# Kernel tuning notes

Hardware: AMD Instinct MI355X
Metric: run time of the kernel (lower is better)

The kernel has to match this reference:

```python
import jax, jax.numpy as jnp
import numpy as np

DIM = 256; NH = 8; WH = 8; WW = 8; N = WH * WW
B, T, M, H, W = 2, 4, 5, 64, 64
HD = DIM // NH
SCALE = HD ** -0.5

def _rel_pos_index():
    coords = np.stack(np.meshgrid(np.arange(WH), np.arange(WW), indexing='ij'))
    cf = coords.reshape(2, -1)
    rc = (cf[:, :, None] - cf[:, None, :]).transpose(1, 2, 0)
    rc[:, :, 0] += WH - 1
    rc[:, :, 1] += WW - 1
    rc[:, :, 0] *= 2 * WW - 1
    return rc.sum(-1)  # (N, N) ints in [0, (2WH-1)(2WW-1))

RPI = _rel_pos_index()

def layer_norm(x, g, b, eps=1e-5):
    mu = x.mean(-1, keepdims=True)
    var = jnp.mean((x - mu) ** 2, axis=-1, keepdims=True)
    return (x - mu) * jax.lax.rsqrt(var + eps) * g + b

def setup_inputs():
    key = jax.random.key(0)
    ks = jax.random.split(key, 32)
    C = DIM
    w = lambda i, shape, s=0.02: jax.random.normal(ks[i], shape, jnp.float32) * s
    return {
        'x': jax.random.normal(ks[0], (B, T, H, W, C), jnp.float32),
        'kv': jax.random.normal(ks[1], (B, M, H, W, C), jnp.float32),
        'mask_matrix': jnp.zeros(((H // WH) * (W // WW), N, N), jnp.float32),
        'norm_q_g': jnp.ones((C,), jnp.float32), 'norm_q_b': jnp.zeros((C,), jnp.float32),
        'norm_kv_g': jnp.ones((C,), jnp.float32), 'norm_kv_b': jnp.zeros((C,), jnp.float32),
        'q_w': w(2, (C, C)), 'q_b': w(3, (C,)),
        'kv_w': w(4, (2 * C, C)), 'kv_b': w(5, (2 * C,)),
        'rpb_table': w(6, ((2 * WH - 1) * (2 * WW - 1), NH)),
        'pos_emb': jax.random.normal(ks[7], (N, C), jnp.float32) / C ** 0.5,
        'pq_w': w(8, (C, C)), 'pq_b': w(9, (C,)),
        'pk_w': w(10, (C, C)), 'pk_b': w(11, (C,)),
        'pv_w': w(12, (C, C)), 'pv_b': w(13, (C,)),
        'po_w': w(14, (C, C)), 'po_b': w(15, (C,)),
        'proj_w': w(16, (C, C)), 'proj_b': w(17, (C,)),
        'norm2_g': jnp.ones((C,), jnp.float32), 'norm2_b': jnp.zeros((C,), jnp.float32),
        'mlp_w1': w(18, (4 * C, C)), 'mlp_b1': w(19, (4 * C,)),
        'mlp_w2': w(20, (C, 4 * C)), 'mlp_b2': w(21, (C,)),
    }

def _attention_pool(xw, pos_emb, pq_w, pq_b, pk_w, pk_b, pv_w, pv_b, po_w, po_b):
    # CLIP-style attention pooling: xw (b, M, N, C) -> (b, N, C)
    b, m, n, C = xw.shape
    avg = xw.mean(axis=1, keepdims=True)
    xw = jnp.concatenate([avg, xw], axis=1) + pos_emb[None, None]  # (b, M+1, N, C)
    tok = xw.reshape(b, (m + 1) * n, C)  # flattened (m n) token axis
    q = (tok[:, :n] @ pq_w.T + pq_b).reshape(b, n, NH, HD).transpose(0, 2, 1, 3) * HD ** -0.5
    k = (tok @ pk_w.T + pk_b).reshape(b, -1, NH, HD).transpose(0, 2, 1, 3)
    v = (tok @ pv_w.T + pv_b).reshape(b, -1, NH, HD).transpose(0, 2, 1, 3)
    a = jax.nn.softmax(jnp.einsum('bhqd,bhkd->bhqk', q, k), axis=-1)
    o = jnp.einsum('bhqk,bhkd->bhqd', a, v).transpose(0, 2, 1, 3).reshape(b, n, C)
    return o @ po_w.T + po_b

def reference(x, kv, mask_matrix, norm_q_g, norm_q_b, norm_kv_g, norm_kv_b,
              q_w, q_b, kv_w, kv_b, rpb_table, pos_emb,
              pq_w, pq_b, pk_w, pk_b, pv_w, pv_b, po_w, po_b,
              proj_w, proj_b, norm2_g, norm2_b, mlp_w1, mlp_b1, mlp_w2, mlp_b2):
    Bv, Tv, Hv, Wv, C = x.shape
    Mv = kv.shape[1]
    nWh, nWw = Hv // WH, Wv // WW
    nW = nWh * nWw
    B_ = Bv * nW
    shortcut = x
    xq = layer_norm(x, norm_q_g, norm_q_b)
    xk = layer_norm(kv, norm_kv_g, norm_kv_b)

    def part(z, S):  # window partition (B,S,H,W,C) -> (B*nW, S, N, C)
        z = z.reshape(Bv, S, nWh, WH, nWw, WW, C)
        return z.transpose(0, 2, 4, 1, 3, 5, 6).reshape(B_, S, N, C)

    qw = part(xq, Tv)
    kvw = part(xk, Mv)
    q = (qw @ q_w.T + q_b).reshape(B_, Tv, N, NH, HD).transpose(0, 1, 3, 2, 4)   # (B_,T,h,N,d)
    kvp = (kvw @ kv_w.T + kv_b).reshape(B_, Mv, N, 2, NH, HD)
    k = kvp[:, :, :, 0].transpose(0, 1, 3, 2, 4)                                  # (B_,M,h,N,d)
    v = kvp[:, :, :, 1].transpose(0, 1, 3, 2, 4)
    attn = jnp.einsum('bthnd,bmhkd->btmhnk', q * SCALE, k)                        # (B_,T,M,h,N,N)
    rpb = rpb_table[RPI.reshape(-1)].reshape(N, N, NH).transpose(2, 0, 1)         # (h,N,N)
    attn = jax.nn.softmax(attn + rpb[None, None, None], axis=-1)  # shift=(0,0) -> mask_matrix unused
    out = jnp.einsum('btmhnk,bmhkd->btmhnd', attn, v)                             # (B_,T,M,h,N,d)
    # faithful to torch: transpose(1,2) (swap T/M) then flat reshape to (B_,T,M,N,C)
    out = out.transpose(0, 2, 1, 3, 4, 5).reshape(B_, Tv, Mv, N, C)
    out = out.reshape(B_ * Tv, Mv, N, C)
    out = _attention_pool(out, pos_emb, pq_w, pq_b, pk_w, pk_b, pv_w, pv_b, po_w, po_b)
    out = out.reshape(B_, Tv, N, C)
    out = jax.nn.gelu(out, approximate=False)
    out = out @ proj_w.T + proj_b
    # window reverse -> (B,T,H,W,C)
    out = out.reshape(Bv, nWh, nWw, Tv, WH, WW, C).transpose(0, 3, 1, 4, 2, 5, 6).reshape(Bv, Tv, Hv, Wv, C)
    x1 = shortcut + out
    h = layer_norm(x1, norm2_g, norm2_b)
    h = jax.nn.gelu(h @ mlp_w1.T + mlp_b1, approximate=False) @ mlp_w2.T + mlp_b2
    return x1 + h
```

## Files before the change

kernel.cpp:

```cpp
#include <hip/hip_runtime.h>
#include <hip/hip_bf16.h>
#include <cstddef>
#include <cstdint>

#define SCALE_QK 0.17677669529663687f

typedef __attribute__((ext_vector_type(8))) short bf16x8;
typedef __attribute__((ext_vector_type(4))) float f32x4;

__global__ __launch_bounds__(256) void convb_kernel(
    const float* __restrict__ src, __hip_bfloat16* __restrict__ dst, int n) {
  int i = blockIdx.x * 256 + threadIdx.x;
  if (i < n) dst[i] = __float2bfloat16(src[i]);
}

__global__ __launch_bounds__(256) void ln_part_kernel(
    const float* __restrict__ in, __hip_bfloat16* __restrict__ out,
    const float* __restrict__ gamma, const float* __restrict__ beta,
    int S, int b0) {
  int r = blockIdx.x;
  int n = r & 63;
  int tmp = r >> 6;
  int s = tmp % S;
  int b_ = b0 + tmp / S;
  int b  = b_ >> 6;
  int wh = (b_ >> 3) & 7;
  int ww = b_ & 7;
  int gh = wh * 8 + (n >> 3);
  int gw = ww * 8 + (n & 7);
  const float* src = in + (((size_t)(b * S + s) * 64 + gh) * 64 + gw) * 256;
  int c = threadIdx.x;
  float v = src[c];
  __shared__ float red[256];
  red[c] = v; __syncthreads();
  for (int off = 128; off > 0; off >>= 1) { if (c < off) red[c] += red[c + off]; __syncthreads(); }
  float mu = red[0] * (1.f / 256.f);
  __syncthreads();
  float dv = v - mu;
  red[c] = dv * dv; __syncthreads();
  for (int off = 128; off > 0; off >>= 1) { if (c < off) red[c] += red[c + off]; __syncthreads(); }
  float var = red[0] * (1.f / 256.f);
  out[(size_t)r * 256 + c] = __float2bfloat16(dv * rsqrtf(var + 1e-5f) * gamma[c] + beta[c]);
}

__global__ __launch_bounds__(256) void ln_plain_kernel(
    const float* __restrict__ in, __hip_bfloat16* __restrict__ out,
    const float* __restrict__ gamma, const float* __restrict__ beta) {
  int r = blockIdx.x;
  const float* src = in + (size_t)r * 256;
  int c = threadIdx.x;
  float v = src[c];
  __shared__ float red[256];
  red[c] = v; __syncthreads();
  for (int off = 128; off > 0; off >>= 1) { if (c < off) red[c] += red[c + off]; __syncthreads(); }
  float mu = red[0] * (1.f / 256.f);
  __syncthreads();
  float dv = v - mu;
  red[c] = dv * dv; __syncthreads();
  for (int off = 128; off > 0; off >>= 1) { if (c < off) red[c] += red[c + off]; __syncthreads(); }
  float var = red[0] * (1.f / 256.f);
  out[(size_t)r * 256 + c] = __float2bfloat16(dv * rsqrtf(var + 1e-5f) * gamma[c] + beta[c]);
}

__global__ __launch_bounds__(256) void mgemm_kernel(
    const ushort* __restrict__ A, const ushort* __restrict__ W,
    const float* __restrict__ bias, const float* __restrict__ resid,
    void* __restrict__ Cp, int Mrows, int N, int K, int flags) {
  __shared__ ushort As[128 * 64];
  __shared__ ushort Bs[128 * 64];
  int tid = threadIdx.x;
  int lane = tid & 63, wid = tid >> 6;
  int wm = wid >> 1, wn = wid & 1;
  int row0 = blockIdx.y * 128, col0 = blockIdx.x * 128;
  int srow = tid >> 3;
  int slot = tid & 7;
  f32x4 acc[4][4];
  #pragma unroll
  for (int m = 0; m < 4; ++m)
    #pragma unroll
    for (int n = 0; n < 4; ++n) acc[m][n] = (f32x4){0.f, 0.f, 0.f, 0.f};

  for (int k0 = 0; k0 < K; k0 += 64) {
    #pragma unroll
    for (int i = 0; i < 4; ++i) {
      int r = i * 32 + srow;
      int gr = row0 + r; if (gr >= Mrows) gr = Mrows - 1;
      bf16x8 va = *(const bf16x8*)(A + (size_t)gr * K + k0 + slot * 8);
      int gc = col0 + r;
      bf16x8 vb = *(const bf16x8*)(W + (size_t)gc * K + k0 + slot * 8);
      int ldso = r * 64 + ((slot ^ (r & 7)) << 3);
      *(bf16x8*)(As + ldso) = va;
      *(bf16x8*)(Bs + ldso) = vb;
    }
    __syncthreads();
    #pragma unroll
    for (int ks = 0; ks < 2; ++ks) {
      bf16x8 af[4], bfr[4];
      int sgrp = ks * 4 + (lane >> 4);
      #pragma unroll
      for (int m = 0; m < 4; ++m) {
        int r = wm * 64 + m * 16 + (lane & 15);
        af[m] = *(const bf16x8*)(As + r * 64 + ((sgrp ^ (r & 7)) << 3));
      }
      #pragma unroll
      for (int n = 0; n < 4; ++n) {
        int r = wn * 64 + n * 16 + (lane & 15);
        bfr[n] = *(const bf16x8*)(Bs + r * 64 + ((sgrp ^ (r & 7)) << 3));
      }
      #pragma unroll
      for (int m = 0; m < 4; ++m)
        #pragma unroll
        for (int n = 0; n < 4; ++n)
          acc[m][n] = __builtin_amdgcn_mfma_f32_16x16x32_bf16(af[m], bfr[n], acc[m][n], 0, 0, 0);
    }
    __syncthreads();
  }

  float* Cf = (float*)Cp;
  __hip_bfloat16* Cb = (__hip_bfloat16*)Cp;
  #pragma unroll
  for (int m = 0; m < 4; ++m) {
    #pragma unroll
    for (int n = 0; n < 4; ++n) {
      int col = col0 + wn * 64 + n * 16 + (lane & 15);
      #pragma unroll
      for (int r = 0; r < 4; ++r) {
        int row = row0 + wm * 64 + m * 16 + (lane >> 4) * 4 + r;
        if (row >= Mrows) continue;
        float v = acc[m][n][r] + (bias ? bias[col] : 0.f);
        if (flags & 1) v = 0.5f * v * (1.f + erff(v * 0.70710678118654752f));
        if (resid) v += resid[(size_t)row * N + col];
        if (flags & 2) Cb[(size_t)row * N + col] = __float2bfloat16(v);
        else           Cf[(size_t)row * N + col] = v;
      }
    }
  }
}

#define TBM 64
#define TBN 64
#define TBK 16
__global__ __launch_bounds__(256) void gemm_kernel(
    const float* __restrict__ A, const float* __restrict__ Wt,
    const float* __restrict__ bias, float* __restrict__ Cc,
    int Mrows, int Nout, int K) {
  __shared__ float Asl[TBK][TBM + 1];
  __shared__ float Wsl[TBK][TBN + 1];
  int tid = threadIdx.x;
  int tx = tid & 15, ty = tid >> 4;
  int row0 = blockIdx.y * TBM, col0 = blockIdx.x * TBN;
  float acc[4][4] = {};
  for (int k0 = 0; k0 < K; k0 += TBK) {
    #pragma unroll
    for (int t = 0; t < 4; ++t) {
      int idx = t * 256 + tid;
      int lm = idx >> 4, lk = idx & 15;
      int gr = row0 + lm;
      Asl[lk][lm] = (gr < Mrows) ? A[(size_t)gr * K + k0 + lk] : 0.f;
      int gc = col0 + lm;
      Wsl[lk][lm] = (gc < Nout) ? Wt[(size_t)gc * K + k0 + lk] : 0.f;
    }
    __syncthreads();
    #pragma unroll
    for (int kk = 0; kk < TBK; ++kk) {
      float a[4], b[4];
      #pragma unroll
      for (int i = 0; i < 4; ++i) a[i] = Asl[kk][ty * 4 + i];
      #pragma unroll
      for (int j = 0; j < 4; ++j) b[j] = Wsl[kk][tx * 4 + j];
      #pragma unroll
      for (int i = 0; i < 4; ++i)
        #pragma unroll
        for (int j = 0; j < 4; ++j)
          acc[i][j] = fmaf(a[i], b[j], acc[i][j]);
    }
    __syncthreads();
  }
  #pragma unroll
  for (int i = 0; i < 4; ++i) {
    int gr = row0 + ty * 4 + i;
    if (gr >= Mrows) continue;
    #pragma unroll
    for (int j = 0; j < 4; ++j) {
      int gc = col0 + tx * 4 + j;
      if (gc >= Nout) continue;
      Cc[(size_t)gr * Nout + gc] = acc[i][j] + bias[gc];
    }
  }
}

__global__ __launch_bounds__(256) void wattn_kernel(
    const float* __restrict__ qb, const float* __restrict__ kvp,
    const float* __restrict__ rpb_table, __hip_bfloat16* __restrict__ xw) {
  int idx = blockIdx.x;
  int h = idx & 7; idx >>= 3;
  int m = idx % 5;
  int b_l = idx / 5;
  int tid = threadIdx.x;
  int n = tid & 63;
  int w = tid >> 6;

  __shared__ float4 ks4[64][9];
  __shared__ float4 vs4[64][9];
  __shared__ float rpbs[64][65];

  {
    int sr = tid >> 2, dg = tid & 3;
    const float* base = kvp + (((size_t)(b_l * 5 + m) * 64 + sr) * 512) + h * 32 + dg * 8;
    float4 k0 = *(const float4*)(base);
    float4 k1 = *(const float4*)(base + 4);
    float4 v0 = *(const float4*)(base + 256);
    float4 v1 = *(const float4*)(base + 260);
    ks4[sr][dg * 2]     = k0;
    ks4[sr][dg * 2 + 1] = k1;
    vs4[sr][dg * 2]     = v0;
    vs4[sr][dg * 2 + 1] = v1;
  }
  for (int e = tid; e < 4096; e += 256) {
    int nn = e >> 6, jj = e & 63;
    int i1 = nn >> 3, j1 = nn & 7, i2 = jj >> 3, j2 = jj & 7;
    rpbs[nn][jj] = rpb_table[((i1 - i2 + 7) * 15 + (j1 - j2 + 7)) * 8 + h];
  }

  float qr[32];
  {
    const float* qrow = qb + (((size_t)(b_l * 4 + w) * 64 + n) * 256) + h * 32;
    #pragma unroll
    for (int i = 0; i < 8; ++i) {
      float4 qv = *(const float4*)(qrow + i * 4);
      qr[i*4+0] = qv.x * SCALE_QK; qr[i*4+1] = qv.y * SCALE_QK;
      qr[i*4+2] = qv.z * SCALE_QK; qr[i*4+3] = qv.w * SCALE_QK;
    }
  }
  __syncthreads();

  float s[64];
  float mx = -1e30f;
  #pragma unroll
  for (int j = 0; j < 64; ++j) {
    float a = 0.f;
    #pragma unroll
    for (int i = 0; i < 8; ++i) {
      float4 kk = ks4[j][i];
      a = fmaf(qr[i*4+0], kk.x, a);
      a = fmaf(qr[i*4+1], kk.y, a);
      a = fmaf(qr[i*4+2], kk.z, a);
      a = fmaf(qr[i*4+3], kk.w, a);
    }
    a += rpbs[n][j];
    s[j] = a;
    mx = fmaxf(mx, a);
  }

  float l = 0.f;
  float acc[32];
  #pragma unroll
  for (int d = 0; d < 32; ++d) acc[d] = 0.f;
  #pragma unroll
  for (int j = 0; j < 64; ++j) {
    float p = __expf(s[j] - mx);
    l += p;
    #pragma unroll
    for (int i = 0; i < 8; ++i) {
      float4 vv = vs4[j][i];
      acc[i*4+0] = fmaf(p, vv.x, acc[i*4+0]);
      acc[i*4+1] = fmaf(p, vv.y, acc[i*4+1]);
      acc[i*4+2] = fmaf(p, vv.z, acc[i*4+2]);
      acc[i*4+3] = fmaf(p, vv.w, acc[i*4+3]);
    }
  }
  float inv = 1.f / l;

  int f = m * 4 + w;
  int tp = f / 5, mp = f % 5;
  int np = h * 8 + (n >> 3);
  int cp = (n & 7) * 32;
  size_t base = ((((size_t)(b_l * 4 + tp) * 5 + mp) * 64 + np) * 256) + cp;
  #pragma unroll
  for (int d = 0; d < 32; ++d) xw[base + d] = __float2bfloat16(acc[d] * inv);
}

__global__ __launch_bounds__(256) void avg3_kernel(
    const __hip_bfloat16* __restrict__ xw, const float* __restrict__ pk,
    const float* __restrict__ pv, const float* __restrict__ pos_emb,
    __hip_bfloat16* __restrict__ avgq, float* __restrict__ pka,
    float* __restrict__ pva) {
  int gid = blockIdx.x * 256 + threadIdx.x;
  int c = gid & 255;
  int rn = gid >> 8;
  int n = rn & 63;
  int bp = rn >> 6;
  size_t base = ((size_t)bp * 320 + n) * 256 + c;
  const size_t stride = 64 * 256;
  float sq = 0.f, sk = 0.f, sv = 0.f;
  #pragma unroll
  for (int m = 0; m < 5; ++m) {
    sq += __bfloat162float(xw[base + m * stride]);
    sk += pk[base + m * stride];
    sv += pv[base + m * stride];
  }
  avgq[(size_t)rn * 256 + c] = __float2bfloat16(sq * 0.2f + pos_emb[n * 256 + c]);
  pka[(size_t)rn * 256 + c] = sk * 0.2f;
  pva[(size_t)rn * 256 + c] = sv * 0.2f;
}

__global__ __launch_bounds__(256) void pattn_kernel(
    const float* __restrict__ pq, const float* __restrict__ pk,
    const float* __restrict__ pv, const float* __restrict__ pka,
    const float* __restrict__ pva, const float* __restrict__ pos_pk,
    const float* __restrict__ pos_pv, __hip_bfloat16* __restrict__ o) {
  int h = blockIdx.x & 7;
  int bp = blockIdx.x >> 3;
  int tid = threadIdx.x;
  int lane = tid & 63;
  int w = tid >> 6;
  __shared__ float4 ks4[64][9];
  __shared__ float4 vs4[64][9];
  __shared__ float sm[4][64];
  __shared__ float sl[4][64];
  __shared__ float sacc[4][64][32];

  int sr = tid >> 2, dg = tid & 3;
  const float* ppkp = pos_pk + sr * 256 + h * 32 + dg * 8;
  const float* ppvp = pos_pv + sr * 256 + h * 32 + dg * 8;
  float4 ppk0 = *(const float4*)(ppkp);
  float4 ppk1 = *(const float4*)(ppkp + 4);
  float4 ppv0 = *(const float4*)(ppvp);
  float4 ppv1 = *(const float4*)(ppvp + 4);

  float qr[32];
  {
    const float* qrow = pq + (((size_t)bp * 64 + lane) * 256) + h * 32;
    #pragma unroll
    for (int i = 0; i < 8; ++i) {
      float4 qv = *(const float4*)(qrow + i * 4);
      qr[i*4+0] = qv.x * SCALE_QK; qr[i*4+1] = qv.y * SCALE_QK;
      qr[i*4+2] = qv.z * SCALE_QK; qr[i*4+3] = qv.w * SCALE_QK;
    }
  }

  float mx = -1e30f, l = 0.f;
  float acc[32];
  #pragma unroll
  for (int d = 0; d < 32; ++d) acc[d] = 0.f;

  for (int mm = 0; mm < 6; ++mm) {
    const float* kr;
    const float* vr;
    if (mm == 0) {
      kr = pka + (((size_t)bp * 64 + sr) * 256) + h * 32 + dg * 8;
      vr = pva + (((size_t)bp * 64 + sr) * 256) + h * 32 + dg * 8;
    } else {
      kr = pk + (((size_t)(bp * 5 + mm - 1) * 64 + sr) * 256) + h * 32 + dg * 8;
      vr = pv + (((size_t)(bp * 5 + mm - 1) * 64 + sr) * 256) + h * 32 + dg * 8;
    }
    __syncthreads();
    {
      float4 a0 = *(const float4*)(kr);
      float4 a1 = *(const float4*)(kr + 4);
      float4 b0 = *(const float4*)(vr);
      float4 b1 = *(const float4*)(vr + 4);
      ks4[sr][dg*2]   = make_float4(a0.x+ppk0.x, a0.y+ppk0.y, a0.z+ppk0.z, a0.w+ppk0.w);
      ks4[sr][dg*2+1] = make_float4(a1.x+ppk1.x, a1.y+ppk1.y, a1.z+ppk1.z, a1.w+ppk1.w);
      vs4[sr][dg*2]   = make_float4(b0.x+ppv0.x, b0.y+ppv0.y, b0.z+ppv0.z, b0.w+ppv0.w);
      vs4[sr][dg*2+1] = make_float4(b1.x+ppv1.x, b1.y+ppv1.y, b1.z+ppv1.z, b1.w+ppv1.w);
    }
    __syncthreads();

    float s[16];
    float cmx = mx;
    #pragma unroll
    for (int jj = 0; jj < 16; ++jj) {
      int j = w * 16 + jj;
      float a = 0.f;
      #pragma unroll
      for (int i = 0; i < 8; ++i) {
        float4 kk = ks4[j][i];
        a = fmaf(qr[i*4+0], kk.x, a);
        a = fmaf(qr[i*4+1], kk.y, a);
        a = fmaf(qr[i*4+2], kk.z, a);
        a = fmaf(qr[i*4+3], kk.w, a);
      }
      s[jj] = a;
      cmx = fmaxf(cmx, a);
    }
    float scale = __expf(mx - cmx);
    l *= scale;
    #pragma unroll
    for (int d = 0; d < 32; ++d) acc[d] *= scale;
    #pragma unroll
    for (int jj = 0; jj < 16; ++jj) {
      int j = w * 16 + jj;
      float p = __expf(s[jj] - cmx);
      l += p;
      #pragma unroll
      for (int i = 0; i < 8; ++i) {
        float4 vv = vs4[j][i];
        acc[i*4+0] = fmaf(p, vv.x, acc[i*4+0]);
        acc[i*4+1] = fmaf(p, vv.y, acc[i*4+1]);
        acc[i*4+2] = fmaf(p, vv.z, acc[i*4+2]);
        acc[i*4+3] = fmaf(p, vv.w, acc[i*4+3]);
      }
    }
    mx = cmx;
  }

  sm[w][lane] = mx;
  sl[w][lane] = l;
  #pragma unroll
  for (int d = 0; d < 32; ++d) sacc[w][lane][d] = acc[d];
  __syncthreads();

  float M = fmaxf(fmaxf(sm[0][lane], sm[1][lane]), fmaxf(sm[2][lane], sm[3][lane]));
  float e0 = __expf(sm[0][lane] - M);
  float e1 = __expf(sm[1][lane] - M);
  float e2 = __expf(sm[2][lane] - M);
  float e3 = __expf(sm[3][lane] - M);
  float L = sl[0][lane]*e0 + sl[1][lane]*e1 + sl[2][lane]*e2 + sl[3][lane]*e3;
  float inv = 1.f / L;
  size_t base = (((size_t)bp * 64 + lane) * 256) + h * 32 + w * 8;
  #pragma unroll
  for (int dd = 0; dd < 8; ++dd) {
    int d = w * 8 + dd;
    float sv = sacc[0][lane][d]*e0 + sacc[1][lane][d]*e1
             + sacc[2][lane][d]*e2 + sacc[3][lane][d]*e3;
    o[base + dd] = __float2bfloat16(sv * inv);
  }
}

__global__ __launch_bounds__(256) void scatter_kernel(
    const float* __restrict__ x, const float* __restrict__ prj,
    float* __restrict__ out, int b0) {
  int gid = blockIdx.x * 256 + threadIdx.x;
  int c = gid & 255;
  int r = gid >> 8;
  int n = r & 63;
  int t = (r >> 6) & 3;
  int b_l = r >> 8;
  int b_ = b0 + b_l;
  int b = b_ >> 6, wh = (b_ >> 3) & 7, ww = b_ & 7;
  int gh = wh * 8 + (n >> 3), gw = ww * 8 + (n & 7);
  size_t pix = (((size_t)(b * 4 + t) * 64 + gh) * 64 + gw) * 256 + c;
  out[pix] = x[pix] + prj[(size_t)r * 256 + c];
}

extern "C" void kernel_launch(void* const* d_in, const int* in_sizes, int n_in,
                              void* d_out, int out_size, void* d_ws, size_t ws_size,
                              hipStream_t stream) {
  const float* x       = (const float*)d_in[0];
  const float* kv      = (const float*)d_in[1];
  const float* nq_g    = (const float*)d_in[3];
  const float* nq_b    = (const float*)d_in[4];
  const float* nk_g    = (const float*)d_in[5];
  const float* nk_b    = (const float*)d_in[6];
  const float* q_w     = (const float*)d_in[7];
  const float* q_b     = (const float*)d_in[8];
  const float* kv_w    = (const float*)d_in[9];
  const float* kv_b    = (const float*)d_in[10];
  const float* rpb     = (const float*)d_in[11];
  const float* pos_emb = (const float*)d_in[12];
  const float* pq_w    = (const float*)d_in[13];
  const float* pq_b    = (const float*)d_in[14];
  const float* pk_w    = (const float*)d_in[15];
  const float* pk_b    = (const float*)d_in[16];
  const float* pv_w    = (const float*)d_in[17];
  const float* pv_b    = (const float*)d_in[18];
  const float* po_w    = (const float*)d_in[19];
  const float* po_b    = (const float*)d_in[20];
  const float* proj_w  = (const float*)d_in[21];
  const float* proj_b  = (const float*)d_in[22];
  const float* n2_g    = (const float*)d_in[23];
  const float* n2_b    = (const float*)d_in[24];
  const float* mlp_w1  = (const float*)d_in[25];
  const float* mlp_b1  = (const float*)d_in[26];
  const float* mlp_w2  = (const float*)d_in[27];
  const float* mlp_b2  = (const float*)d_in[28];
  float* out = (float*)d_out;
  float* ws = (float*)d_ws;

  size_t wsF = ws_size / sizeof(float);
  float* pospk = ws;
  float* pospv = ws + 16384;
  __hip_bfloat16* wq_b    = (__hip_bfloat16*)(ws + 32768);
  __hip_bfloat16* wkv_b   = (__hip_bfloat16*)(ws + 65536);
  __hip_bfloat16* wpq_b   = (__hip_bfloat16*)(ws + 131072);
  __hip_bfloat16* wpk_b   = (__hip_bfloat16*)(ws + 163840);
  __hip_bfloat16* wpv_b   = (__hip_bfloat16*)(ws + 196608);
  __hip_bfloat16* wpo_b   = (__hip_bfloat16*)(ws + 229376);
  __hip_bfloat16* wproj_b = (__hip_bfloat16*)(ws + 262144);
  __hip_bfloat16* wm1_b   = (__hip_bfloat16*)(ws + 294912);
  __hip_bfloat16* wm2_b   = (__hip_bfloat16*)(ws + 425984);
  const size_t FIXED = 557056;

  int CH = 0;
  const int cands[7] = {64, 32, 16, 8, 4, 2, 1};
  for (int i = 0; i < 7; ++i) {
    size_t need = FIXED + (size_t)1179648 * cands[i];
    if (need <= wsF) { CH = cands[i]; break; }
  }
  if (CH == 0) return;
  size_t CHs = (size_t)CH;
  float* cb = ws + FIXED;

  __hip_bfloat16* qw_b  = (__hip_bfloat16*)cb;
  __hip_bfloat16* kvw_b = (__hip_bfloat16*)(cb + 32768 * CHs);
  float* qb2 = cb + 73728 * CHs;
  float* kvp = cb + 139264 * CHs;
  float* PK  = cb;
  float* PV  = cb + 327680 * CHs;
  __hip_bfloat16* xw_b  = (__hip_bfloat16*)(cb + 655360 * CHs);
  __hip_bfloat16* AVG_b = (__hip_bfloat16*)(cb + 819200 * CHs);
  float* PQ  = cb + 851968 * CHs;
  float* PKA = cb + 917504 * CHs;
  float* PVA = cb + 983040 * CHs;
  __hip_bfloat16* OC_b = (__hip_bfloat16*)(cb + 1048576 * CHs);
  __hip_bfloat16* PG_b = (__hip_bfloat16*)(cb + 1081344 * CHs);
  float* PRJ = cb + 1114112 * CHs;

  gemm_kernel<<<dim3(4, 1), 256, 0, stream>>>(pos_emb, pk_w, pk_b, pospk, 64, 256, 256);
  gemm_kernel<<<dim3(4, 1), 256, 0, stream>>>(pos_emb, pv_w, pv_b, pospv, 64, 256, 256);
  convb_kernel<<<256,  256, 0, stream>>>(q_w,    wq_b,    65536);
  convb_kernel<<<512,  256, 0, stream>>>(kv_w,   wkv_b,   131072);
  convb_kernel<<<256,  256, 0, stream>>>(pq_w,   wpq_b,   65536);
  convb_kernel<<<256,  256, 0, stream>>>(pk_w,   wpk_b,   65536);
  convb_kernel<<<256,  256, 0, stream>>>(pv_w,   wpv_b,   65536);
  convb_kernel<<<256,  256, 0, stream>>>(po_w,   wpo_b,   65536);
  convb_kernel<<<256,  256, 0, stream>>>(proj_w, wproj_b, 65536);
  convb_kernel<<<1024, 256, 0, stream>>>(mlp_w1, wm1_b,   262144);
  convb_kernel<<<1024, 256, 0, stream>>>(mlp_w2, wm2_b,   262144);

  for (int c0 = 0; c0 < 128; c0 += CH) {
    int rowsQ  = CH * 256;
    int rowsKV = CH * 320;
    int rowsXW = CH * 1280;
    int bpC    = CH * 4;
    int rowsP  = bpC * 64;
    ln_part_kernel<<<rowsQ, 256, 0, stream>>>(x, qw_b, nq_g, nq_b, 4, c0);
    ln_part_kernel<<<rowsKV, 256, 0, stream>>>(kv, kvw_b, nk_g, nk_b, 5, c0);
    mgemm_kernel<<<dim3(2, rowsQ / 128), 256, 0, stream>>>(
        (const ushort*)qw_b, (const ushort*)wq_b, q_b, nullptr, qb2, rowsQ, 256, 256, 0);
    mgemm_kernel<<<dim3(4, (rowsKV + 127) / 128), 256, 0, stream>>>(
        (const ushort*)kvw_b, (const ushort*)wkv_b, kv_b, nullptr, kvp, rowsKV, 512, 256, 0);
    wattn_kernel<<<CH * 40, 256, 0, stream>>>(qb2, kvp, rpb, xw_b);
    mgemm_kernel<<<dim3(2, rowsXW / 128), 256, 0, stream>>>(
        (const ushort*)xw_b, (const ushort*)wpk_b, nullptr, nullptr, PK, rowsXW, 256, 256, 0);
    mgemm_kernel<<<dim3(2, rowsXW / 128), 256, 0, stream>>>(
        (const ushort*)xw_b, (const ushort*)wpv_b, nullptr, nullptr, PV, rowsXW, 256, 256, 0);
    avg3_kernel<<<rowsP, 256, 0, stream>>>(xw_b, PK, PV, pos_emb, AVG_b, PKA, PVA);
    mgemm_kernel<<<dim3(2, rowsP / 128), 256, 0, stream>>>(
        (const ushort*)AVG_b, (const ushort*)wpq_b, pq_b, nullptr, PQ, rowsP, 256, 256, 0);
    pattn_kernel<<<bpC * 8, 256, 0, stream>>>(PQ, PK, PV, PKA, PVA, pospk, pospv, OC_b);
    mgemm_kernel<<<dim3(2, rowsP / 128), 256, 0, stream>>>(
        (const ushort*)OC_b, (const ushort*)wpo_b, po_b, nullptr, PG_b, rowsP, 256, 256, 3);
    mgemm_kernel<<<dim3(2, rowsP / 128), 256, 0, stream>>>(
        (const ushort*)PG_b, (const ushort*)wproj_b, proj_b, nullptr, PRJ, rowsP, 256, 256, 0);
    scatter_kernel<<<rowsP, 256, 0, stream>>>(x, PRJ, out, c0);
  }

  int R = 32768;
  while ((size_t)R * 640 > (size_t)1179648 * CHs && R > 128) R >>= 1;
  __hip_bfloat16* ln2c = (__hip_bfloat16*)cb;
  __hip_bfloat16* h1c  = (__hip_bfloat16*)(cb + 128 * (size_t)R);
  for (int r0 = 0; r0 < 32768; r0 += R) {
    ln_plain_kernel<<<R, 256, 0, stream>>>(out + (size_t)r0 * 256, ln2c, n2_g, n2_b);
    mgemm_kernel<<<dim3(8, R / 128), 256, 0, stream>>>(
        (const ushort*)ln2c, (const ushort*)wm1_b, mlp_b1, nullptr, h1c, R, 1024, 256, 3);
    mgemm_kernel<<<dim3(2, R / 128), 256, 0, stream>>>(
        (const ushort*)h1c, (const ushort*)wm2_b, mlp_b2, out + (size_t)r0 * 256,
        out + (size_t)r0 * 256, R, 256, 1024, 0);
  }
}
```

Before: 2.173 ms.

## Precompute bf16 bias table and use online softmax in window attention

A new setup kernel expands the relative-position bias table into a per-head 64x64 bf16 array once, so window attention copies it into shared memory instead of gathering from the table. The bias shared buffer shrinks from float to bf16. The score/softmax loop becomes an online softmax over four 16-key chunks, which avoids keeping all 64 scores in registers and should raise occupancy. The QK dot product also uses two partial accumulators for more instruction-level parallelism. Costs are extra rescale work per chunk and reduced bias precision.

```diff
diff --git a/kernel.cpp b/kernel.cpp
--- a/kernel.cpp
+++ b/kernel.cpp
@@ -12,6 +12,18 @@
     const float* __restrict__ src, __hip_bfloat16* __restrict__ dst, int n) {
   int i = blockIdx.x * 256 + threadIdx.x;
   if (i < n) dst[i] = __float2bfloat16(src[i]);
+}
+
+__global__ __launch_bounds__(256) void rpbx_kernel(
+    const float* __restrict__ rpb_table, ushort* __restrict__ rpbx) {
+  int gid = blockIdx.x * 256 + threadIdx.x;
+  int h = gid >> 12;
+  int rest = gid & 4095;
+  int n = rest >> 6, j = rest & 63;
+  int i1 = n >> 3, j1 = n & 7, i2 = j >> 3, j2 = j & 7;
+  float v = rpb_table[((i1 - i2 + 7) * 15 + (j1 - j2 + 7)) * 8 + h];
+  __hip_bfloat16 b = __float2bfloat16(v);
+  rpbx[gid] = *reinterpret_cast<ushort*>(&b);
 }
 
 __global__ __launch_bounds__(256) void ln_part_kernel(
@@ -191,7 +203,7 @@
 
 __global__ __launch_bounds__(256) void wattn_kernel(
     const float* __restrict__ qb, const float* __restrict__ kvp,
-    const float* __restrict__ rpb_table, __hip_bfloat16* __restrict__ xw) {
+    const ushort* __restrict__ rpbx, __hip_bfloat16* __restrict__ xw) {
   int idx = blockIdx.x;
   int h = idx & 7; idx >>= 3;
   int m = idx % 5;
@@ -202,7 +214,7 @@
 
   __shared__ float4 ks4[64][9];
   __shared__ float4 vs4[64][9];
-  __shared__ float rpbs[64][65];
+  __shared__ ushort rpbs[64][65];
 
   {
     int sr = tid >> 2, dg = tid & 3;
@@ -216,10 +228,10 @@
     vs4[sr][dg * 2]     = v0;
     vs4[sr][dg * 2 + 1] = v1;
   }
-  for (int e = tid; e < 4096; e += 256) {
-    int nn = e >> 6, jj = e & 63;
-    int i1 = nn >> 3, j1 = nn & 7, i2 = jj >> 3, j2 = jj & 7;
-    rpbs[nn][jj] = rpb_table[((i1 - i2 + 7) * 15 + (j1 - j2 + 7)) * 8 + h];
+  {
+    const ushort* rsrc = rpbx + h * 4096;
+    #pragma unroll
+    for (int e = tid; e < 4096; e += 256) rpbs[e >> 6][e & 63] = rsrc[e];
   }
 
   float qr[32];
@@ -234,40 +246,57 @@
   }
   __syncthreads();
 
-  float s[64];
-  float mx = -1e30f;
-  #pragma unroll
-  for (int j = 0; j < 64; ++j) {
-    float a = 0.f;
-    #pragma unroll
-    for (int i = 0; i < 8; ++i) {
-      float4 kk = ks4[j][i];
-      a = fmaf(qr[i*4+0], kk.x, a);
-      a = fmaf(qr[i*4+1], kk.y, a);
-      a = fmaf(qr[i*4+2], kk.z, a);
-      a = fmaf(qr[i*4+3], kk.w, a);
-    }
-    a += rpbs[n][j];
-    s[j] = a;
-    mx = fmaxf(mx, a);
-  }
-
-  float l = 0.f;
+  float mx = -1e30f, l = 0.f;
   float acc[32];
   #pragma unroll
   for (int d = 0; d < 32; ++d) acc[d] = 0.f;
-  #pragma unroll
-  for (int j = 0; j < 64; ++j) {
-    float p = __expf(s[j] - mx);
-    l += p;
-    #pragma unroll
-    for (int i = 0; i < 8; ++i) {
-      float4 vv = vs4[j][i];
-      acc[i*4+0] = fmaf(p, vv.x, acc[i*4+0]);
-      acc[i*4+1] = fmaf(p, vv.y, acc[i*4+1]);
-      acc[i*4+2] = fmaf(p, vv.z, acc[i*4+2]);
-      acc[i*4+3] = fmaf(p, vv.w, acc[i*4+3]);
-    }
+
+  #pragma unroll
+  for (int st = 0; st < 4; ++st) {
+    float s[16];
+    float cmx = mx;
+    #pragma unroll
+    for (int jj = 0; jj < 16; ++jj) {
+      int j = st * 16 + jj;
+      float a0 = 0.f, a1 = 0.f;
+      #pragma unroll
+      for (int i = 0; i < 4; ++i) {
+        float4 k0 = ks4[j][i * 2];
+        float4 k1 = ks4[j][i * 2 + 1];
+        a0 = fmaf(qr[i*8+0], k0.x, a0);
+        a0 = fmaf(qr[i*8+1], k0.y, a0);
+        a0 = fmaf(qr[i*8+2], k0.z, a0);
+        a0 = fmaf(qr[i*8+3], k0.w, a0);
+        a1 = fmaf(qr[i*8+4], k1.x, a1);
+        a1 = fmaf(qr[i*8+5], k1.y, a1);
+        a1 = fmaf(qr[i*8+6], k1.z, a1);
+        a1 = fmaf(qr[i*8+7], k1.w, a1);
+      }
+      ushort rb = rpbs[n][j];
+      float bias = __bfloat162float(*reinterpret_cast<__hip_bfloat16*>(&rb));
+      float sb = a0 + a1 + bias;
+      s[jj] = sb;
+      cmx = fmaxf(cmx, sb);
+    }
+    float sc = __expf(mx - cmx);
+    l *= sc;
+    #pragma unroll
+    for (int d = 0; d < 32; ++d) acc[d] *= sc;
+    #pragma unroll
+    for (int jj = 0; jj < 16; ++jj) {
+      int j = st * 16 + jj;
+      float p = __expf(s[jj] - cmx);
+      l += p;
+      #pragma unroll
+      for (int i = 0; i < 8; ++i) {
+        float4 vv = vs4[j][i];
+        acc[i*4+0] = fmaf(p, vv.x, acc[i*4+0]);
+        acc[i*4+1] = fmaf(p, vv.y, acc[i*4+1]);
+        acc[i*4+2] = fmaf(p, vv.z, acc[i*4+2]);
+        acc[i*4+3] = fmaf(p, vv.w, acc[i*4+3]);
+      }
+    }
+    mx = cmx;
   }
   float inv = 1.f / l;
 
@@ -490,7 +519,8 @@
   __hip_bfloat16* wproj_b = (__hip_bfloat16*)(ws + 262144);
   __hip_bfloat16* wm1_b   = (__hip_bfloat16*)(ws + 294912);
   __hip_bfloat16* wm2_b   = (__hip_bfloat16*)(ws + 425984);
-  const size_t FIXED = 557056;
+  ushort* rpbx            = (ushort*)(ws + 557056);
+  const size_t FIXED = 573440;
 
   int CH = 0;
   const int cands[7] = {64, 32, 16, 8, 4, 2, 1};
@@ -519,6 +549,7 @@
 
   gemm_kernel<<<dim3(4, 1), 256, 0, stream>>>(pos_emb, pk_w, pk_b, pospk, 64, 256, 256);
   gemm_kernel<<<dim3(4, 1), 256, 0, stream>>>(pos_emb, pv_w, pv_b, pospv, 64, 256, 256);
+  rpbx_kernel<<<128, 256, 0, stream>>>(rpb, rpbx);
   convb_kernel<<<256,  256, 0, stream>>>(q_w,    wq_b,    65536);
   convb_kernel<<<512,  256, 0, stream>>>(kv_w,   wkv_b,   131072);
   convb_kernel<<<256,  256, 0, stream>>>(pq_w,   wpq_b,   65536);
@@ -541,7 +572,7 @@
         (const ushort*)qw_b, (const ushort*)wq_b, q_b, nullptr, qb2, rowsQ, 256, 256, 0);
     mgemm_kernel<<<dim3(4, (rowsKV + 127) / 128), 256, 0, stream>>>(
         (const ushort*)kvw_b, (const ushort*)wkv_b, kv_b, nullptr, kvp, rowsKV, 512, 256, 0);
-    wattn_kernel<<<CH * 40, 256, 0, stream>>>(qb2, kvp, rpb, xw_b);
+    wattn_kernel<<<CH * 40, 256, 0, stream>>>(qb2, kvp, rpbx, xw_b);
     mgemm_kernel<<<dim3(2, rowsXW / 128), 256, 0, stream>>>(
         (const ushort*)xw_b, (const ushort*)wpk_b, nullptr, nullptr, PK, rowsXW, 256, 256, 0);
     mgemm_kernel<<<dim3(2, rowsXW / 128), 256, 0, stream>>>(
```

After: 1.846 ms. 1.18x faster.
